# Kernel optimization log

Hardware: AMD Instinct MI355X
Metric: run time of the kernel (lower is better)

Reference implementation:

```python
import jax, jax.numpy as jnp
import numpy as np

B, N, E, D, H, C, FF, NQ, NCLS = 4, 1024, 512, 256, 2, 128, 1024, 4, 24
K_LOCAL, K_GLOBAL = 8, 7


def _ln(x, g, b, eps=1e-5):
    m = jnp.mean(x, -1, keepdims=True)
    v = jnp.mean((x - m) ** 2, -1, keepdims=True)
    return (x - m) * jax.lax.rsqrt(v + eps) * g + b


def _knn_mask(dist, k, exclude_self):
    # dist: [n, n]; returns bool mask[target, source] of k nearest sources per target
    n = dist.shape[-1]
    d = jnp.where(jnp.eye(n, dtype=bool), 1e9, dist) if exclude_self else dist
    idx = jax.lax.top_k(-d, k)[1]  # [n, k]
    rows = jnp.arange(n)[:, None]
    return jnp.zeros((n, n), dtype=bool).at[rows, idx].set(True)


def _mha(q, k, v, scale, extra_mask=None):
    # q: [B,Lq,H,C]  k,v: [B,Lk,H,C]
    logits = jnp.einsum('bqhc,bkhc->bhqk', q, k) * scale
    if extra_mask is not None:
        logits = logits + extra_mask
    a = jax.nn.softmax(logits, axis=-1)
    return jnp.einsum('bhqk,bkhc->bqhc', a, v)


def _forward(inputs, cellposes, sparse_rand, emb_W, emb_b, pe_tab, pe_W1, pe_b1, pe_W2, pe_b2,
             gat_W, gat_att_src, gat_att_dst, gat_b, ln_g, ln_b,
             tf_qkv_W, tf_qkv_b, tf_out_W, tf_out_b, tf_ff1_W, tf_ff1_b, tf_ff2_W, tf_ff2_b,
             tf_ln1_g, tf_ln1_b, tf_ln2_g, tf_ln2_b,
             query_embed, pool_in_W, pool_in_b, pool_out_W, pool_out_b,
             m1_W, m1_b, m_ln1_g, m_ln1_b, m2_W, m2_b, m_ln2_g, m_ln2_b, m3_W, m3_b,
             c1_W, c1_b, c2_W, c2_b, c3_W, c3_b, c4_W, c4_b, masks):
    # masks are all ones (full bags) -> key_padding_mask is all-False, no padding effect
    x = inputs @ emb_W.T + emb_b                                  # [B,N,D]
    # 2D position embedding: per-coordinate Embedding -> Linear -> ReLU -> Linear
    pos_idx = jnp.clip(cellposes, 0, 1000).astype(jnp.int32)      # [B,N,2]
    pes = []
    for c in range(2):
        e = pe_tab[c][pos_idx[..., c]]                            # [B,N,D//2]
        e = jax.nn.relu(e @ pe_W1[c].T + pe_b1[c]) @ pe_W2[c].T + pe_b2[c]
        pes.append(e)
    x = x + jnp.concatenate(pes, axis=-1)
    # kNN graph: local k=8 with self-loops + global k=7 without; coalesce('max') => edge-set union
    pm = cellposes.mean(axis=1, keepdims=True)
    ps = cellposes.std(axis=1, keepdims=True) + 1e-8
    pn = (cellposes - pm) / ps
    sq = jnp.sum((pn[:, :, None, :] - pn[:, None, :, :]) ** 2, axis=-1)
    dist = jax.lax.stop_gradient(jnp.sqrt(sq + 1e-12))            # [B,N,N]
    local = jax.vmap(lambda d: _knn_mask(d, K_LOCAL, False))(dist)
    glob = jax.vmap(lambda d: _knn_mask(d, K_GLOBAL, True))(dist)
    adj = local | glob                                            # [B, target, source]
    # GAT layers (PyG GATConv; edge weights are ignored since edge_dim=None)
    for l in range(gat_W.shape[0]):
        res = x
        h = (x @ gat_W[l].T).reshape(B, N, H, C)
        a_src = jnp.einsum('bnhc,hc->bnh', h, gat_att_src[l])
        a_dst = jnp.einsum('bnhc,hc->bnh', h, gat_att_dst[l])
        e = jax.nn.leaky_relu(a_dst[:, :, None, :] + a_src[:, None, :, :], 0.2)  # [B,t,s,H]
        e = jnp.where(adj[..., None], e, -1e9)
        a = jax.nn.softmax(e, axis=2)
        out = jnp.einsum('btsh,bshc->bthc', a, h).reshape(B, N, D) + gat_b[l]
        x = _ln(out + res, ln_g, ln_b)
    # TransformerEncoder: post-norm, ReLU FFN, batch_first, eval (no dropout)
    scale = 1.0 / jnp.sqrt(jnp.float32(C))
    for l in range(tf_qkv_W.shape[0]):
        qkv = x @ tf_qkv_W[l].T + tf_qkv_b[l]
        q, k, v = [t.reshape(B, N, H, C) for t in jnp.split(qkv, 3, axis=-1)]
        o = _mha(q, k, v, scale).reshape(B, N, D) @ tf_out_W[l].T + tf_out_b[l]
        x = _ln(x + o, tf_ln1_g[l], tf_ln1_b[l])
        ff = jax.nn.relu(x @ tf_ff1_W[l].T + tf_ff1_b[l]) @ tf_ff2_W[l].T + tf_ff2_b[l]
        x = _ln(x + ff, tf_ln2_g[l], tf_ln2_b[l])
    x = _ln(x, ln_g, ln_b)
    pooled_avg = x.mean(axis=1)                                   # AdaptiveAvgPool1d(1) == mean over seq
    # Sparse multihead attention pooling with learned queries
    queries = jnp.broadcast_to(query_embed[None], (B, NQ, D))
    attn_mask = jnp.where(sparse_rand < 0.3, 0.0, -1e9)           # [NQ, N]
    Wq, Wk, Wv = jnp.split(pool_in_W, 3, axis=0)
    bq, bk, bv = jnp.split(pool_in_b, 3, axis=0)
    q = (queries @ Wq.T + bq).reshape(B, NQ, H, C)
    k = (x @ Wk.T + bk).reshape(B, N, H, C)
    v = (x @ Wv.T + bv).reshape(B, N, H, C)
    pooled_att = _mha(q, k, v, scale, attn_mask[None, None]).reshape(B, NQ, D) @ pool_out_W.T + pool_out_b
    combined = jnp.concatenate([pooled_avg, pooled_att.reshape(B, NQ * D)], axis=-1)  # [B,(1+NQ)*D]
    h = jax.nn.relu(combined @ m1_W.T + m1_b)
    h = _ln(h, m_ln1_g, m_ln1_b)
    h = jax.nn.relu(h @ m2_W.T + m2_b)
    h = _ln(h, m_ln2_g, m_ln2_b)
    h = h @ m3_W.T + m3_b
    h = jax.nn.relu(h @ c1_W.T + c1_b)
    h = jax.nn.relu(h @ c2_W.T + c2_b)
    h = jax.nn.relu(h @ c3_W.T + c3_b)
    return h @ c4_W.T + c4_b                                      # [B, num_classes]


def setup_inputs() -> dict:
    key = jax.random.key(0)
    ks = iter(jax.random.split(key, 80))
    def W(shape, s=0.02):
        return jax.random.normal(next(ks), shape, jnp.float32) * s
    z = lambda *s: jnp.zeros(s, jnp.float32)
    o = lambda *s: jnp.ones(s, jnp.float32)
    return dict(
        inputs=jax.random.normal(next(ks), (B, N, E), jnp.float32),
        cellposes=jax.random.uniform(next(ks), (B, N, 2), jnp.float32) * 1000.0,
        sparse_rand=jax.random.uniform(next(ks), (NQ, N), jnp.float32),
        emb_W=W((D, E)), emb_b=z(D),
        pe_tab=W((2, 1001, D // 2)), pe_W1=W((2, D // 2, D // 2)), pe_b1=z(2, D // 2),
        pe_W2=W((2, D // 2, D // 2)), pe_b2=z(2, D // 2),
        gat_W=W((2, D, D)), gat_att_src=W((2, H, C)), gat_att_dst=W((2, H, C)), gat_b=z(2, D),
        ln_g=o(D), ln_b=z(D),
        tf_qkv_W=W((2, 3 * D, D)), tf_qkv_b=z(2, 3 * D), tf_out_W=W((2, D, D)), tf_out_b=z(2, D),
        tf_ff1_W=W((2, FF, D)), tf_ff1_b=z(2, FF), tf_ff2_W=W((2, D, FF)), tf_ff2_b=z(2, D),
        tf_ln1_g=o(2, D), tf_ln1_b=z(2, D), tf_ln2_g=o(2, D), tf_ln2_b=z(2, D),
        query_embed=W((NQ, D)),
        pool_in_W=W((3 * D, D)), pool_in_b=z(3 * D), pool_out_W=W((D, D)), pool_out_b=z(D),
        m1_W=W((1024, (1 + NQ) * D)), m1_b=z(1024), m_ln1_g=o(1024), m_ln1_b=z(1024),
        m2_W=W((1024, 1024)), m2_b=z(1024), m_ln2_g=o(1024), m_ln2_b=z(1024),
        m3_W=W((1024, 1024)), m3_b=z(1024),
        c1_W=W((1032, 1024)), c1_b=z(1032), c2_W=W((512, 1032)), c2_b=z(512),
        c3_W=W((256, 512)), c3_b=z(256), c4_W=W((NCLS, 256)), c4_b=z(NCLS),
        masks=jnp.ones((B, N), jnp.int32),
    )


def reference(inputs, cellposes, sparse_rand, emb_W, emb_b, pe_tab, pe_W1, pe_b1, pe_W2, pe_b2,
              gat_W, gat_att_src, gat_att_dst, gat_b, ln_g, ln_b,
              tf_qkv_W, tf_qkv_b, tf_out_W, tf_out_b, tf_ff1_W, tf_ff1_b, tf_ff2_W, tf_ff2_b,
              tf_ln1_g, tf_ln1_b, tf_ln2_g, tf_ln2_b,
              query_embed, pool_in_W, pool_in_b, pool_out_W, pool_out_b,
              m1_W, m1_b, m_ln1_g, m_ln1_b, m2_W, m2_b, m_ln2_g, m_ln2_b, m3_W, m3_b,
              c1_W, c1_b, c2_W, c2_b, c3_W, c3_b, c4_W, c4_b, masks):
    return _forward(inputs, cellposes, sparse_rand, emb_W, emb_b, pe_tab, pe_W1, pe_b1, pe_W2, pe_b2,
                    gat_W, gat_att_src, gat_att_dst, gat_b, ln_g, ln_b,
                    tf_qkv_W, tf_qkv_b, tf_out_W, tf_out_b, tf_ff1_W, tf_ff1_b, tf_ff2_W, tf_ff2_b,
                    tf_ln1_g, tf_ln1_b, tf_ln2_g, tf_ln2_b,
                    query_embed, pool_in_W, pool_in_b, pool_out_W, pool_out_b,
                    m1_W, m1_b, m_ln1_g, m_ln1_b, m2_W, m2_b, m_ln2_g, m_ln2_b, m3_W, m3_b,
                    c1_W, c1_b, c2_W, c2_b, c3_W, c3_b, c4_W, c4_b, masks)
```

## Files before the change

kernel.cpp:

```cpp
#include <hip/hip_runtime.h>
#include <hip/hip_bf16.h>


typedef __bf16 bf16x8 __attribute__((ext_vector_type(8)));
typedef float  f32x4  __attribute__((ext_vector_type(4)));

__device__ __forceinline__ ushort f2b(float f) {
  __hip_bfloat16 h = __float2bfloat16(f);
  return *(ushort*)&h;
}
__device__ __forceinline__ float b2f(ushort u) {
  union { unsigned i; float f; } v; v.i = ((unsigned)u) << 16; return v.f;
}

__device__ __forceinline__ float blk_sum256(float v, float* red) {
  int t = threadIdx.x;
  red[t] = v; __syncthreads();
  #pragma unroll
  for (int off = 128; off > 0; off >>= 1) {
    if (t < off) red[t] += red[t + off];
    __syncthreads();
  }
  float r = red[0]; __syncthreads();
  return r;
}

__device__ __forceinline__ void stage8(const ushort* __restrict__ src, ushort* dst) {
  *(uint4*)dst = *(const uint4*)src;
}
__device__ __forceinline__ void stage8(const float* __restrict__ src, ushort* dst) {
  float4 a = ((const float4*)src)[0];
  float4 b = ((const float4*)src)[1];
  ushort4 o0, o1;
  o0.x = f2b(a.x); o0.y = f2b(a.y); o0.z = f2b(a.z); o0.w = f2b(a.w);
  o1.x = f2b(b.x); o1.y = f2b(b.y); o1.z = f2b(b.z); o1.w = f2b(b.w);
  *(ushort4*)dst = o0;
  *(ushort4*)(dst + 4) = o1;
}

template<typename CT, typename AT, typename WT, bool VSPLIT, bool GATS>
__global__ __launch_bounds__(256) void mfma_gemm(
    const AT* __restrict__ A, int lda,
    const WT* __restrict__ Bw, int ldb,
    const float* __restrict__ bias,
    CT* __restrict__ C, int ldc, int K, int relu,
    ushort* __restrict__ VT,
    const float* __restrict__ asrcW, const float* __restrict__ adstW,
    float* __restrict__ ASRC, float* __restrict__ ADST)
{
  __shared__ ushort As[64][40];
  __shared__ ushort Bs[128][40];
  int tid = threadIdx.x;
  int lane = tid & 63, wave = tid >> 6;
  int wm = wave >> 1, wn = wave & 1;
  int quad = lane >> 4, l16 = lane & 15;
  long mBase = blockIdx.y * 64, nBase = blockIdx.x * 128;

  f32x4 zero4 = {0.f, 0.f, 0.f, 0.f};
  f32x4 acc[2][4];
  #pragma unroll
  for (int i = 0; i < 2; i++)
    #pragma unroll
    for (int j = 0; j < 4; j++) acc[i][j] = zero4;

  for (int k0 = 0; k0 < K; k0 += 32) {
    {
      int r = tid >> 2, sg = (tid & 3) * 8;
      stage8(A + (mBase + r) * lda + k0 + sg, &As[r][sg]);
    }
    #pragma unroll
    for (int p = 0; p < 2; p++) {
      int idx = p * 256 + tid;
      int r = idx >> 2, sg = (idx & 3) * 8;
      stage8(Bw + (nBase + r) * ldb + k0 + sg, &Bs[r][sg]);
    }
    __syncthreads();
    bf16x8 af[2], bfr[4];
    #pragma unroll
    for (int i = 0; i < 2; i++)
      af[i] = *(const bf16x8*)&As[wm * 32 + i * 16 + l16][quad * 8];
    #pragma unroll
    for (int j = 0; j < 4; j++)
      bfr[j] = *(const bf16x8*)&Bs[wn * 64 + j * 16 + l16][quad * 8];
    #pragma unroll
    for (int i = 0; i < 2; i++)
      #pragma unroll
      for (int j = 0; j < 4; j++)
        acc[i][j] = __builtin_amdgcn_mfma_f32_16x16x32_bf16(af[i], bfr[j], acc[i][j], 0, 0, 0);
    __syncthreads();
  }
  #pragma unroll
  for (int i = 0; i < 2; i++) {
    #pragma unroll
    for (int j = 0; j < 4; j++) {
      long col = nBase + wn * 64 + j * 16 + l16;
      float bv = bias ? bias[col] : 0.f;
      long row0 = mBase + wm * 32 + i * 16 + quad * 4;
      if (VSPLIT && col >= 512) {
        int cm = (int)col - 512, hh = cm >> 7, cc = cm & 127;
        long bidx = row0 >> 10, n0 = row0 & 1023;
        ushort4 o;
        o.x = f2b(acc[i][j][0] + bv);
        o.y = f2b(acc[i][j][1] + bv);
        o.z = f2b(acc[i][j][2] + bv);
        o.w = f2b(acc[i][j][3] + bv);
        *(ushort4*)&VT[(((bidx * 2 + hh) * 128 + cc) << 10) + n0] = o;
      } else {
        #pragma unroll
        for (int r = 0; r < 4; r++) {
          float v = acc[i][j][r] + bv;
          if (relu) v = fmaxf(v, 0.f);
          if constexpr (sizeof(CT) == 2) C[(row0 + r) * ldc + col] = f2b(v);
          else                           C[(row0 + r) * ldc + col] = v;
        }
      }
    }
  }
  if constexpr (GATS) {
    __shared__ float RS[64][2], RD[64][2];
    float ps[2][4], pd[2][4];
    #pragma unroll
    for (int i = 0; i < 2; i++)
      #pragma unroll
      for (int r = 0; r < 4; r++) { ps[i][r] = 0.f; pd[i][r] = 0.f; }
    #pragma unroll
    for (int j = 0; j < 4; j++) {
      long col = nBase + wn * 64 + j * 16 + l16;
      float ws = asrcW[col], wd = adstW[col];
      #pragma unroll
      for (int i = 0; i < 2; i++)
        #pragma unroll
        for (int r = 0; r < 4; r++) {
          ps[i][r] += acc[i][j][r] * ws;
          pd[i][r] += acc[i][j][r] * wd;
        }
    }
    #pragma unroll
    for (int off = 1; off < 16; off <<= 1)
      #pragma unroll
      for (int i = 0; i < 2; i++)
        #pragma unroll
        for (int r = 0; r < 4; r++) {
          ps[i][r] += __shfl_xor(ps[i][r], off);
          pd[i][r] += __shfl_xor(pd[i][r], off);
        }
    if (l16 == 0) {
      #pragma unroll
      for (int i = 0; i < 2; i++)
        #pragma unroll
        for (int r = 0; r < 4; r++) {
          int row = wm * 32 + i * 16 + quad * 4 + r;
          RS[row][wn] = ps[i][r];
          RD[row][wn] = pd[i][r];
        }
    }
    __syncthreads();
    if (tid < 64) {
      long gr = mBase + tid;
      ASRC[gr * 2 + blockIdx.x] = RS[tid][0] + RS[tid][1];
      ADST[gr * 2 + blockIdx.x] = RD[tid][0] + RD[tid][1];
    }
  }
}

template<typename CT, typename AT, typename WT>
static void mgemm(hipStream_t st, const AT* A, int lda, const WT* B, int ldb,
                  const float* bias, CT* C, int ldc, int M, int N, int K, int relu) {
  dim3 grid(N / 128, M / 64);
  mfma_gemm<CT, AT, WT, false, false><<<grid, 256, 0, st>>>(
      A, lda, B, ldb, bias, C, ldc, K, relu, nullptr, nullptr, nullptr, nullptr, nullptr);
}
template<typename AT, typename WT>
static void mgemm_vt(hipStream_t st, const AT* A, int lda, const WT* B, int ldb,
                     const float* bias, ushort* C, int ldc, int M, int N, int K, ushort* VT) {
  dim3 grid(N / 128, M / 64);
  mfma_gemm<ushort, AT, WT, true, false><<<grid, 256, 0, st>>>(
      A, lda, B, ldb, bias, C, ldc, K, 0, VT, nullptr, nullptr, nullptr, nullptr);
}
template<typename AT, typename WT>
static void mgemm_gat(hipStream_t st, const AT* A, int lda, const WT* B, int ldb,
                      float* C, int ldc, int M, int N, int K,
                      const float* asrcW, const float* adstW, float* AS, float* AD) {
  dim3 grid(N / 128, M / 64);
  mfma_gemm<float, AT, WT, false, true><<<grid, 256, 0, st>>>(
      A, lda, B, ldb, nullptr, C, ldc, K, 0, nullptr, asrcW, adstW, AS, AD);
}

__global__ __launch_bounds__(256) void pos_mlp(
    const float* __restrict__ cellp, const float* __restrict__ tab,
    const float* __restrict__ W1, const float* __restrict__ b1,
    const float* __restrict__ W2, const float* __restrict__ b2,
    float* __restrict__ X, ushort* __restrict__ Xb)
{
  __shared__ ushort Es[64][136];
  __shared__ ushort Bs[128][136];
  __shared__ ushort H1s[64][136];
  int tid = threadIdx.x;
  int lane = tid & 63, wave = tid >> 6;
  int wm = wave >> 1, wn = wave & 1;
  int quad = lane >> 4, l16 = lane & 15;
  int r0 = blockIdx.x * 64, c = blockIdx.y;

  #pragma unroll
  for (int p = 0; p < 4; p++) {
    int idx = p * 256 + tid;
    int r = idx >> 4, c8 = (idx & 15) * 8;
    float pos = cellp[(r0 + r) * 2 + c];
    pos = fminf(fmaxf(pos, 0.f), 1000.f);
    int pi = (int)pos;
    stage8(tab + ((long)(c * 1001 + pi)) * 128 + c8, &Es[r][c8]);
  }
  #pragma unroll
  for (int p = 0; p < 8; p++) {
    int idx = p * 256 + tid;
    int r = idx >> 4, c8 = (idx & 15) * 8;
    stage8(W1 + ((long)(c * 128 + r)) * 128 + c8, &Bs[r][c8]);
  }
  __syncthreads();

  f32x4 zero4 = {0.f, 0.f, 0.f, 0.f};
  f32x4 acc[2][4];
  #pragma unroll
  for (int i = 0; i < 2; i++)
    #pragma unroll
    for (int j = 0; j < 4; j++) acc[i][j] = zero4;
  #pragma unroll
  for (int ks = 0; ks < 4; ks++) {
    bf16x8 af[2], bfr[4];
    #pragma unroll
    for (int i = 0; i < 2; i++)
      af[i] = *(const bf16x8*)&Es[wm * 32 + i * 16 + l16][ks * 32 + quad * 8];
    #pragma unroll
    for (int j = 0; j < 4; j++)
      bfr[j] = *(const bf16x8*)&Bs[wn * 64 + j * 16 + l16][ks * 32 + quad * 8];
    #pragma unroll
    for (int i = 0; i < 2; i++)
      #pragma unroll
      for (int j = 0; j < 4; j++)
        acc[i][j] = __builtin_amdgcn_mfma_f32_16x16x32_bf16(af[i], bfr[j], acc[i][j], 0, 0, 0);
  }
  #pragma unroll
  for (int i = 0; i < 2; i++)
    #pragma unroll
    for (int j = 0; j < 4; j++) {
      int col = wn * 64 + j * 16 + l16;
      float bv = b1[c * 128 + col];
      #pragma unroll
      for (int r = 0; r < 4; r++) {
        int row = wm * 32 + i * 16 + quad * 4 + r;
        H1s[row][col] = f2b(fmaxf(acc[i][j][r] + bv, 0.f));
      }
    }
  __syncthreads();
  #pragma unroll
  for (int p = 0; p < 8; p++) {
    int idx = p * 256 + tid;
    int r = idx >> 4, c8 = (idx & 15) * 8;
    stage8(W2 + ((long)(c * 128 + r)) * 128 + c8, &Bs[r][c8]);
  }
  __syncthreads();
  #pragma unroll
  for (int i = 0; i < 2; i++)
    #pragma unroll
    for (int j = 0; j < 4; j++) acc[i][j] = zero4;
  #pragma unroll
  for (int ks = 0; ks < 4; ks++) {
    bf16x8 af[2], bfr[4];
    #pragma unroll
    for (int i = 0; i < 2; i++)
      af[i] = *(const bf16x8*)&H1s[wm * 32 + i * 16 + l16][ks * 32 + quad * 8];
    #pragma unroll
    for (int j = 0; j < 4; j++)
      bfr[j] = *(const bf16x8*)&Bs[wn * 64 + j * 16 + l16][ks * 32 + quad * 8];
    #pragma unroll
    for (int i = 0; i < 2; i++)
      #pragma unroll
      for (int j = 0; j < 4; j++)
        acc[i][j] = __builtin_amdgcn_mfma_f32_16x16x32_bf16(af[i], bfr[j], acc[i][j], 0, 0, 0);
  }
  #pragma unroll
  for (int i = 0; i < 2; i++)
    #pragma unroll
    for (int j = 0; j < 4; j++) {
      int col = wn * 64 + j * 16 + l16;
      float bv = b2[c * 128 + col];
      #pragma unroll
      for (int r = 0; r < 4; r++) {
        long row = r0 + wm * 32 + i * 16 + quad * 4 + r;
        long idx = row * 256 + c * 128 + col;
        float v = X[idx] + (acc[i][j][r] + bv);
        X[idx] = v;
        Xb[idx] = f2b(v);
      }
    }
}

template<int M_>
__global__ __launch_bounds__(256) void skinny_gemm(
    const float* __restrict__ A, int lda,
    const float* __restrict__ W, int K,
    float* __restrict__ P, int N, int slice)
{
  __shared__ float Asl[M_ * 192];
  __shared__ float Pr[4][M_][64];
  int tid = threadIdx.x;
  int ks = blockIdx.y;
  int kbeg = ks * slice;
  int kend = min(K, kbeg + slice);
  int sl = kend - kbeg;
  for (int idx = tid; idx < M_ * sl; idx += 256) {
    int m = idx / sl, k = idx - m * sl;
    Asl[m * sl + k] = A[(long)m * lda + kbeg + k];
  }
  __syncthreads();
  int n = blockIdx.x * 64 + (tid & 63);
  int sub = tid >> 6;
  int sl4 = (sl + 3) >> 2;
  int k0 = kbeg + sub * sl4;
  int k1 = min(kend, k0 + sl4);
  float acc[M_];
  #pragma unroll
  for (int m = 0; m < M_; m++) acc[m] = 0.f;
  if (n < N) {
    const float* wr = W + (long)n * K;
    for (int k = k0; k < k1; k++) {
      float w = wr[k];
      int kl = k - kbeg;
      #pragma unroll
      for (int m = 0; m < M_; m++) acc[m] += w * Asl[m * sl + kl];
    }
  }
  #pragma unroll
  for (int m = 0; m < M_; m++) Pr[sub][m][tid & 63] = acc[m];
  __syncthreads();
  if (sub == 0 && n < N) {
    #pragma unroll
    for (int m = 0; m < M_; m++) {
      float s = Pr[0][m][tid] + Pr[1][m][tid] + Pr[2][m][tid] + Pr[3][m][tid];
      P[((long)(ks * M_ + m)) * N + n] = s;
    }
  }
}

__global__ __launch_bounds__(256) void skinny_epi(
    const float* __restrict__ P, const float* __restrict__ bias,
    float* __restrict__ out, int M, int N, int KS, int relu)
{
  int idx = blockIdx.x * 256 + threadIdx.x;
  if (idx >= M * N) return;
  int m = idx / N, n = idx - m * N;
  float s = bias[n];
  for (int ks = 0; ks < KS; ks++) s += P[((long)(ks * M + m)) * N + n];
  if (relu) s = fmaxf(s, 0.f);
  out[(long)m * N + n] = s;
}

template<int M_>
static void sgemm(hipStream_t st, const float* A, int lda, const float* W, int K,
                  const float* bias, float* out, float* P, int N, int KS, int relu) {
  int slice = (K + KS - 1) / KS;
  dim3 grid((N + 63) / 64, KS);
  skinny_gemm<M_><<<grid, 256, 0, st>>>(A, lda, W, K, P, N, slice);
  skinny_epi<<<(M_ * N + 255) / 256, 256, 0, st>>>(P, bias, out, M_, N, KS, relu);
}

__global__ __launch_bounds__(256) void bag_stats(const float* __restrict__ cp, float* __restrict__ PN) {
  int b = blockIdx.x, tid = threadIdx.x;
  __shared__ float red[256];
  for (int c = 0; c < 2; c++) {
    float s = 0.f;
    for (int n = tid; n < 1024; n += 256) s += cp[((b << 10) + n) * 2 + c];
    float mean = blk_sum256(s, red) * (1.f / 1024.f);
    s = 0.f;
    for (int n = tid; n < 1024; n += 256) { float d = cp[((b << 10) + n) * 2 + c] - mean; s += d * d; }
    float var = blk_sum256(s, red) * (1.f / 1024.f);
    float inv = 1.f / (sqrtf(var) + 1e-8f);
    for (int n = tid; n < 1024; n += 256)
      PN[((b << 10) + n) * 2 + c] = (cp[((b << 10) + n) * 2 + c] - mean) * inv;
  }
}

__global__ __launch_bounds__(256) void knn_sel(const float* __restrict__ PN,
                                               int* __restrict__ NBR) {
  int blk = blockIdx.x;
  int b = blk >> 7, grp = blk & 127;
  int tid = threadIdx.x;
  int wave = tid >> 6, lane = tid & 63;
  __shared__ float px[1024], py[1024];
  for (int i = tid; i < 1024; i += 256) {
    px[i] = PN[((b << 10) + i) * 2 + 0];
    py[i] = PN[((b << 10) + i) * 2 + 1];
  }
  __syncthreads();
  #pragma unroll
  for (int sub = 0; sub < 2; sub++) {
    int t = grp * 8 + wave * 2 + sub;
    float tx = px[t], ty = py[t];
    float dloc[16];
    #pragma unroll
    for (int k = 0; k < 16; k++) {
      int s = lane + (k << 6);
      float dx = __fadd_rn(px[s], -tx), dy = __fadd_rn(py[s], -ty);
      float d2 = __fadd_rn(__fadd_rn(__fmul_rn(dx, dx), __fmul_rn(dy, dy)), 1e-12f);
      dloc[k] = sqrtf(d2);
    }
    int res[8];
    #pragma unroll
    for (int it = 0; it < 8; it++) {
      float bd = dloc[0]; int bk = 0;
      #pragma unroll
      for (int k = 1; k < 16; k++)
        if (dloc[k] < bd) { bd = dloc[k]; bk = k; }
      unsigned long long key =
          (((unsigned long long)__float_as_uint(bd)) << 32) | (unsigned)(lane + (bk << 6));
      #pragma unroll
      for (int off = 1; off < 64; off <<= 1) {
        unsigned long long o = __shfl_xor(key, off);
        if (o < key) key = o;
      }
      int widx = (int)(key & 0xffffffffu);
      res[it] = widx;
      if ((widx & 63) == lane) dloc[widx >> 6] = 3.4e38f;
    }
    if (lane < 8) NBR[((long)((b << 10) + t)) * 8 + lane] = res[lane];
  }
}

__global__ __launch_bounds__(256) void gat_aggr_ln(
    const float* __restrict__ Hh, const float* __restrict__ ASRC, const float* __restrict__ ADST,
    const int* __restrict__ NBR, const float* __restrict__ gbias,
    const float* __restrict__ lng, const float* __restrict__ lnb,
    float* __restrict__ X, ushort* __restrict__ Xb)
{
  int row = blockIdx.x, tid = threadIdx.x;
  int b = row >> 10;
  __shared__ int nb[8];
  __shared__ float w[2][8];
  __shared__ float red[256];
  if (tid < 8) {
    int v = NBR[(long)row * 8 + tid];
    nb[tid] = min(max(v, 0), 1023);
  }
  __syncthreads();
  if (tid < 16) {
    int i = tid & 7, h = tid >> 3;
    float e = ADST[row * 2 + h] + ASRC[((b << 10) + nb[i]) * 2 + h];
    w[h][i] = (e >= 0.f) ? e : 0.2f * e;
  }
  __syncthreads();
  if (tid < 2) {
    float m = -3.4e38f;
    for (int i = 0; i < 8; i++) m = fmaxf(m, w[tid][i]);
    float s = 0.f;
    for (int i = 0; i < 8; i++) { float e = expf(w[tid][i] - m); w[tid][i] = e; s += e; }
    float inv = 1.f / s;
    for (int i = 0; i < 8; i++) w[tid][i] *= inv;
  }
  __syncthreads();
  int h = tid >> 7, c = tid & 127;
  float acc = 0.f;
  #pragma unroll
  for (int i = 0; i < 8; i++)
    acc += w[h][i] * Hh[((long)((b << 10) + nb[i])) * 256 + h * 128 + c];
  float v = acc + gbias[tid] + X[(long)row * 256 + tid];
  float mean = blk_sum256(v, red) * (1.f / 256.f);
  float dv = v - mean;
  float var = blk_sum256(dv * dv, red) * (1.f / 256.f);
  float o = dv * rsqrtf(var + 1e-5f) * lng[tid] + lnb[tid];
  X[(long)row * 256 + tid] = o;
  Xb[(long)row * 256 + tid] = f2b(o);
}

__global__ __launch_bounds__(256) void add_ln4(const float* __restrict__ res,
    const float* __restrict__ Yv, const float* __restrict__ g, const float* __restrict__ b,
    float* __restrict__ out, ushort* __restrict__ outb)
{
  int wave = threadIdx.x >> 6, lane = threadIdx.x & 63;
  long row = blockIdx.x * 4 + wave;
  const float* yr = Yv + row * 256;
  const float* rr = res ? res + row * 256 : nullptr;
  float v[4];
  float s = 0.f;
  #pragma unroll
  for (int i = 0; i < 4; i++) {
    int d = lane + i * 64;
    float x = yr[d];
    if (rr) x += rr[d];
    v[i] = x; s += x;
  }
  #pragma unroll
  for (int off = 32; off > 0; off >>= 1) s += __shfl_xor(s, off);
  float mean = s * (1.f / 256.f);
  float vs = 0.f;
  #pragma unroll
  for (int i = 0; i < 4; i++) { float dv = v[i] - mean; vs += dv * dv; }
  #pragma unroll
  for (int off = 32; off > 0; off >>= 1) vs += __shfl_xor(vs, off);
  float rstd = rsqrtf(vs * (1.f / 256.f) + 1e-5f);
  #pragma unroll
  for (int i = 0; i < 4; i++) {
    int d = lane + i * 64;
    float o = (v[i] - mean) * rstd * g[d] + b[d];
    out[row * 256 + d] = o;
    if (outb) outb[row * 256 + d] = f2b(o);
  }
}

__global__ __launch_bounds__(256) void add_ln_big(const float* __restrict__ Yv,
    const float* __restrict__ g, const float* __restrict__ b,
    float* __restrict__ out)
{
  int row = blockIdx.x, tid = threadIdx.x;
  __shared__ float red[256];
  float vals[4];
  float s = 0.f;
  #pragma unroll
  for (int i = 0; i < 4; i++) {
    int d = tid + (i << 8);
    float v = Yv[(long)row * 1024 + d];
    vals[i] = v; s += v;
  }
  float mean = blk_sum256(s, red) * (1.f / 1024.f);
  s = 0.f;
  #pragma unroll
  for (int i = 0; i < 4; i++) { float dv = vals[i] - mean; s += dv * dv; }
  float var = blk_sum256(s, red) * (1.f / 1024.f);
  float rstd = rsqrtf(var + 1e-5f);
  #pragma unroll
  for (int i = 0; i < 4; i++) {
    int d = tid + (i << 8);
    out[(long)row * 1024 + d] = (vals[i] - mean) * rstd * g[d] + b[d];
  }
}

__global__ __launch_bounds__(256) void flash_mfma(const ushort* __restrict__ QKV,
                                                  const ushort* __restrict__ VT,
                                                  ushort* __restrict__ O)
{
  const float scale = 0.08838834764831845f;
  int blk = blockIdx.x;
  int qt = blk & 15, bh = blk >> 4;
  int b = bh >> 1, h = bh & 1;
  const ushort* qkg = QKV + (long)b * 1024 * 768 + h * 128;
  const ushort* vtg = VT + ((long)bh << 17);

  __shared__ ushort Qs[64][136];
  __shared__ ushort Ks[64][136];
  __shared__ ushort Vt[128][72];
  __shared__ ushort Ps[4][16][72];

  int tid = threadIdx.x;
  int wave = tid >> 6, lane = tid & 63;
  int quad = lane >> 4, l16 = lane & 15;

  #pragma unroll
  for (int p = 0; p < 4; p++) {
    int idx = p * 256 + tid;
    int r = idx >> 4, c8 = (idx & 15) * 8;
    *(uint4*)&Qs[r][c8] = *(const uint4*)(qkg + (long)(qt * 64 + r) * 768 + c8);
  }
  __syncthreads();
  bf16x8 af[4];
  #pragma unroll
  for (int ks = 0; ks < 4; ks++)
    af[ks] = *(const bf16x8*)&Qs[wave * 16 + l16][ks * 32 + quad * 8];

  f32x4 Oacc[8];
  f32x4 zero4 = {0.f, 0.f, 0.f, 0.f};
  #pragma unroll
  for (int j = 0; j < 8; j++) Oacc[j] = zero4;
  float mr[4], lr[4];
  #pragma unroll
  for (int r = 0; r < 4; r++) { mr[r] = -3.4e38f; lr[r] = 0.f; }

  for (int kt = 0; kt < 16; kt++) {
    __syncthreads();
    #pragma unroll
    for (int p = 0; p < 4; p++) {
      int idx = p * 256 + tid;
      int r = idx >> 4, c8 = (idx & 15) * 8;
      *(uint4*)&Ks[r][c8] = *(const uint4*)(qkg + (long)(kt * 64 + r) * 768 + 256 + c8);
      int c = idx >> 3, k8 = (idx & 7) * 8;
      *(uint4*)&Vt[c][k8] = *(const uint4*)(vtg + ((long)c << 10) + kt * 64 + k8);
    }
    __syncthreads();
    f32x4 acc[4];
    #pragma unroll
    for (int j = 0; j < 4; j++) acc[j] = zero4;
    #pragma unroll
    for (int ks = 0; ks < 4; ks++) {
      #pragma unroll
      for (int j = 0; j < 4; j++) {
        bf16x8 kb = *(const bf16x8*)&Ks[j * 16 + l16][ks * 32 + quad * 8];
        acc[j] = __builtin_amdgcn_mfma_f32_16x16x32_bf16(af[ks], kb, acc[j], 0, 0, 0);
      }
    }
    float sv[4][4], tmax[4];
    #pragma unroll
    for (int r = 0; r < 4; r++) tmax[r] = -3.4e38f;
    #pragma unroll
    for (int j = 0; j < 4; j++)
      #pragma unroll
      for (int r = 0; r < 4; r++) {
        float x = acc[j][r] * scale;
        sv[j][r] = x;
        tmax[r] = fmaxf(tmax[r], x);
      }
    #pragma unroll
    for (int off = 1; off < 16; off <<= 1)
      #pragma unroll
      for (int r = 0; r < 4; r++) tmax[r] = fmaxf(tmax[r], __shfl_xor(tmax[r], off));
    float alpha[4], rsum[4];
    #pragma unroll
    for (int r = 0; r < 4; r++) {
      float mn = fmaxf(mr[r], tmax[r]);
      alpha[r] = expf(mr[r] - mn);
      mr[r] = mn;
      rsum[r] = 0.f;
    }
    #pragma unroll
    for (int j = 0; j < 4; j++)
      #pragma unroll
      for (int r = 0; r < 4; r++) {
        float p = expf(sv[j][r] - mr[r]);
        sv[j][r] = p;
        rsum[r] += p;
      }
    #pragma unroll
    for (int off = 1; off < 16; off <<= 1)
      #pragma unroll
      for (int r = 0; r < 4; r++) rsum[r] += __shfl_xor(rsum[r], off);
    #pragma unroll
    for (int r = 0; r < 4; r++) lr[r] = lr[r] * alpha[r] + rsum[r];
    #pragma unroll
    for (int j = 0; j < 4; j++)
      #pragma unroll
      for (int r = 0; r < 4; r++)
        Ps[wave][quad * 4 + r][j * 16 + l16] = f2b(sv[j][r]);
    #pragma unroll
    for (int jj = 0; jj < 8; jj++)
      #pragma unroll
      for (int r = 0; r < 4; r++) Oacc[jj][r] *= alpha[r];
    __syncthreads();
    #pragma unroll
    for (int s = 0; s < 2; s++) {
      bf16x8 pa = *(const bf16x8*)&Ps[wave][l16][s * 32 + quad * 8];
      #pragma unroll
      for (int jj = 0; jj < 8; jj++) {
        bf16x8 vb = *(const bf16x8*)&Vt[jj * 16 + l16][s * 32 + quad * 8];
        Oacc[jj] = __builtin_amdgcn_mfma_f32_16x16x32_bf16(pa, vb, Oacc[jj], 0, 0, 0);
      }
    }
  }
  long row0 = (long)b * 1024 + qt * 64 + wave * 16 + quad * 4;
  #pragma unroll
  for (int jj = 0; jj < 8; jj++) {
    int col = h * 128 + jj * 16 + l16;
    #pragma unroll
    for (int r = 0; r < 4; r++)
      O[(row0 + r) * 256 + col] = f2b(Oacc[jj][r] / lr[r]);
  }
}

__global__ __launch_bounds__(128) void pool_split(
    const float* __restrict__ qe, const float* __restrict__ pinW, const float* __restrict__ pinB,
    const float* __restrict__ srand, const ushort* __restrict__ KV,
    float* __restrict__ PM, float* __restrict__ PL, float* __restrict__ PO)
{
  int cid = blockIdx.x;
  int id = blockIdx.y;
  int h = id & 1, nq = (id >> 1) & 3, b = id >> 3;
  int tid = threadIdx.x;
  __shared__ float qs[128];
  __shared__ float eg[128];
  __shared__ float red[128];
  {
    float a = pinB[h * 128 + tid];
    const float* wr = pinW + ((long)(h * 128 + tid)) * 256;
    const float* qr = qe + nq * 256;
    for (int i = 0; i < 256; i++) a += qr[i] * wr[i];
    qs[tid] = a;
  }
  __syncthreads();
  const float scale = 0.08838834764831845f;
  int s = cid * 128 + tid;
  float d = 0.f;
  {
    const ushort* kr = KV + ((long)((b << 10) + s)) * 512 + h * 128;
    #pragma unroll
    for (int c8 = 0; c8 < 128; c8 += 8) {
      uint4 kv4 = *(const uint4*)(kr + c8);
      const ushort* kp = (const ushort*)&kv4;
      #pragma unroll
      for (int j = 0; j < 8; j++) d += qs[c8 + j] * b2f(kp[j]);
    }
  }
  float lg = d * scale + ((srand[nq * 1024 + s] < 0.3f) ? 0.f : -1e9f);
  red[tid] = lg; __syncthreads();
  for (int off = 64; off > 0; off >>= 1) { if (tid < off) red[tid] = fmaxf(red[tid], red[tid + off]); __syncthreads(); }
  float m = red[0]; __syncthreads();
  float e = expf(lg - m);
  eg[tid] = e;
  red[tid] = e; __syncthreads();
  for (int off = 64; off > 0; off >>= 1) { if (tid < off) red[tid] += red[tid + off]; __syncthreads(); }
  float l = red[0];
  __syncthreads();
  float o = 0.f;
  const ushort* vbase = KV + ((long)((b << 10) + cid * 128)) * 512 + 256 + h * 128 + tid;
  for (int ss = 0; ss < 128; ss++)
    o += eg[ss] * b2f(vbase[(long)ss * 512]);
  int part = id * 8 + cid;
  PO[(long)part * 128 + tid] = o;
  if (tid == 0) { PM[part] = m; PL[part] = l; }
}

__global__ __launch_bounds__(128) void pool_merge(
    const float* __restrict__ PM, const float* __restrict__ PL, const float* __restrict__ PO,
    float* __restrict__ ATTP)
{
  int id = blockIdx.x;
  int h = id & 1, nq = (id >> 1) & 3, b = id >> 3;
  int tid = threadIdx.x;
  float m = -3.4e38f;
  #pragma unroll
  for (int c = 0; c < 8; c++) m = fmaxf(m, PM[id * 8 + c]);
  float l = 0.f, o = 0.f;
  #pragma unroll
  for (int c = 0; c < 8; c++) {
    float w = expf(PM[id * 8 + c] - m);
    l += PL[id * 8 + c] * w;
    o += PO[(long)(id * 8 + c) * 128 + tid] * w;
  }
  ATTP[(b * 4 + nq) * 256 + h * 128 + tid] = o / l;
}

__global__ __launch_bounds__(256) void col_mean_part(const float* __restrict__ X,
                                                     float* __restrict__ PSUM)
{
  int blk = blockIdx.x;
  int b = blk >> 4, ch = blk & 15;
  int d = threadIdx.x;
  float s = 0.f;
  int n0 = ch * 64;
  const float* xr = X + ((long)((b << 10) + n0)) * 256 + d;
  #pragma unroll 4
  for (int n = 0; n < 64; n++) s += xr[(long)n * 256];
  PSUM[(long)blk * 256 + d] = s;
}

__global__ __launch_bounds__(256) void combined_merge(const float* __restrict__ PSUM,
    const float* __restrict__ ATTO, float* __restrict__ CMB)
{
  int b = blockIdx.x, d = threadIdx.x;
  float s = 0.f;
  #pragma unroll
  for (int ch = 0; ch < 16; ch++) s += PSUM[(long)(b * 16 + ch) * 256 + d];
  CMB[b * 1280 + d] = s * (1.f / 1024.f);
  #pragma unroll
  for (int q = 0; q < 4; q++)
    CMB[b * 1280 + 256 + q * 256 + d] = ATTO[(b * 4 + q) * 256 + d];
}

__global__ void store_out(const float* __restrict__ src, float* __restrict__ dst, int n) {
  int i = blockIdx.x * blockDim.x + threadIdx.x;
  if (i < n) dst[i] = src[i];
}
__global__ void fill_out_zero(float* __restrict__ dst, int n) {
  int i = blockIdx.x * blockDim.x + threadIdx.x;
  if (i < n) dst[i] = 0.f;
}

extern "C" void kernel_launch(void* const* d_in, const int* in_sizes, int n_in,
                              void* d_out, int out_size, void* d_ws, size_t ws_size,
                              hipStream_t stream)
{
  const float* inp      = (const float*)d_in[0];
  const float* cellp    = (const float*)d_in[1];
  const float* srand    = (const float*)d_in[2];
  const float* emb_W    = (const float*)d_in[3];
  const float* emb_b    = (const float*)d_in[4];
  const float* pe_tab   = (const float*)d_in[5];
  const float* pe_W1    = (const float*)d_in[6];
  const float* pe_b1    = (const float*)d_in[7];
  const float* pe_W2    = (const float*)d_in[8];
  const float* pe_b2    = (const float*)d_in[9];
  const float* gat_W    = (const float*)d_in[10];
  const float* gat_asrc = (const float*)d_in[11];
  const float* gat_adst = (const float*)d_in[12];
  const float* gat_b    = (const float*)d_in[13];
  const float* ln_g     = (const float*)d_in[14];
  const float* ln_b     = (const float*)d_in[15];
  const float* qkv_W    = (const float*)d_in[16];
  const float* qkv_b    = (const float*)d_in[17];
  const float* out_W    = (const float*)d_in[18];
  const float* out_b    = (const float*)d_in[19];
  const float* ff1_W    = (const float*)d_in[20];
  const float* ff1_b    = (const float*)d_in[21];
  const float* ff2_W    = (const float*)d_in[22];
  const float* ff2_b    = (const float*)d_in[23];
  const float* ln1_g    = (const float*)d_in[24];
  const float* ln1_b    = (const float*)d_in[25];
  const float* ln2_g    = (const float*)d_in[26];
  const float* ln2_b    = (const float*)d_in[27];
  const float* q_emb    = (const float*)d_in[28];
  const float* pin_W    = (const float*)d_in[29];
  const float* pin_b    = (const float*)d_in[30];
  const float* pout_W   = (const float*)d_in[31];
  const float* pout_b   = (const float*)d_in[32];
  const float* m1_W     = (const float*)d_in[33];
  const float* m1_b     = (const float*)d_in[34];
  const float* mln1_g   = (const float*)d_in[35];
  const float* mln1_b   = (const float*)d_in[36];
  const float* m2_W     = (const float*)d_in[37];
  const float* m2_b     = (const float*)d_in[38];
  const float* mln2_g   = (const float*)d_in[39];
  const float* mln2_b   = (const float*)d_in[40];
  const float* m3_W     = (const float*)d_in[41];
  const float* m3_b     = (const float*)d_in[42];
  const float* c1_W     = (const float*)d_in[43];
  const float* c1_b     = (const float*)d_in[44];
  const float* c2_W     = (const float*)d_in[45];
  const float* c2_b     = (const float*)d_in[46];
  const float* c3_W     = (const float*)d_in[47];
  const float* c3_b     = (const float*)d_in[48];
  const float* c4_W     = (const float*)d_in[49];
  const float* c4_b     = (const float*)d_in[50];
  (void)in_sizes; (void)n_in;

  char* base = (char*)d_ws;
  size_t off = 0;
  auto alloc = [&](size_t bytes) { void* p = base + off; off += (bytes + 255) & ~size_t(255); return p; };
  float* PN    = (float*)alloc(32768);
  float* AS    = (float*)alloc(32768);
  float* AD    = (float*)alloc(32768);
  float* ATTP  = (float*)alloc(16384);
  float* ATTO  = (float*)alloc(16384);
  float* CMB   = (float*)alloc(20480);
  float* Ha    = (float*)alloc(16384);
  float* Hb    = (float*)alloc(16384);
  float* Hc    = (float*)alloc(16640);
  float* Hd    = (float*)alloc(8192);
  float* He    = (float*)alloc(4096);
  float* Hf    = (float*)alloc(512);
  float* Pk    = (float*)alloc(262144);
  float* PPM   = (float*)alloc(1024);
  float* PPL   = (float*)alloc(1024);
  float* PPO   = (float*)alloc(131072);
  float* PSUM  = (float*)alloc(65536);
  int*   NBR   = (int*)alloc(131072);
  float* X     = (float*)alloc(4194304);
  ushort* Xb   = (ushort*)alloc(2097152);
  char*  Rq    = (char*)alloc(6291456);
  char*  Rf    = (char*)alloc(4194304);
  float*  F1   = (float*)alloc(4194304);
  ushort* QKVb = (ushort*)Rq;
  float*  F2   = (float*)Rq;
  ushort* KVb  = (ushort*)Rq;
  ushort* Ob   = (ushort*)Rf;
  ushort* VT   = (ushort*)(Rf + 2097152);
  ushort* FFBb = (ushort*)Rf;
  if (ws_size < off) { fill_out_zero<<<1, 128, 0, stream>>>((float*)d_out, out_size); return; }

  bag_stats<<<4, 256, 0, stream>>>(cellp, PN);
  knn_sel<<<512, 256, 0, stream>>>(PN, NBR);

  mgemm<float>(stream, inp, 512, emb_W, 512, emb_b, X, 256, 4096, 256, 512, 0);
  pos_mlp<<<dim3(64, 2), 256, 0, stream>>>(cellp, pe_tab, pe_W1, pe_b1, pe_W2, pe_b2, X, Xb);

  for (int l = 0; l < 2; l++) {
    mgemm_gat(stream, Xb, 256, gat_W + l * 65536, 256, F1, 256, 4096, 256, 256,
              gat_asrc + l * 256, gat_adst + l * 256, AS, AD);
    gat_aggr_ln<<<4096, 256, 0, stream>>>(F1, AS, AD, NBR, gat_b + l * 256, ln_g, ln_b, X, Xb);
  }

  for (int l = 0; l < 2; l++) {
    mgemm_vt(stream, Xb, 256, qkv_W + (long)l * 768 * 256, 256, qkv_b + l * 768,
             QKVb, 768, 4096, 768, 256, VT);
    flash_mfma<<<256, 256, 0, stream>>>(QKVb, VT, Ob);
    mgemm<float>(stream, Ob, 256, out_W + l * 65536, 256, out_b + l * 256, F2, 256,
                 4096, 256, 256, 0);
    add_ln4<<<1024, 256, 0, stream>>>(X, F2, ln1_g + l * 256, ln1_b + l * 256, X, Xb);
    mgemm<ushort>(stream, Xb, 256, ff1_W + l * 262144, 256, ff1_b + l * 1024,
                  FFBb, 1024, 4096, 1024, 256, 1);
    mgemm<float>(stream, FFBb, 1024, ff2_W + l * 262144, 1024, ff2_b + l * 256,
                 F2, 256, 4096, 256, 1024, 0);
    add_ln4<<<1024, 256, 0, stream>>>(X, F2, ln2_g + l * 256, ln2_b + l * 256, X, Xb);
  }

  add_ln4<<<1024, 256, 0, stream>>>((const float*)nullptr, X, ln_g, ln_b, X, Xb);

  mgemm<ushort>(stream, Xb, 256, pin_W + 65536, 256, pin_b + 256, KVb, 512, 4096, 512, 256, 0);
  pool_split<<<dim3(8, 32), 128, 0, stream>>>(q_emb, pin_W, pin_b, srand, KVb, PPM, PPL, PPO);
  pool_merge<<<32, 128, 0, stream>>>(PPM, PPL, PPO, ATTP);
  sgemm<16>(stream, ATTP, 256, pout_W, 256, pout_b, ATTO, Pk, 256, 2, 0);
  col_mean_part<<<64, 256, 0, stream>>>(X, PSUM);
  combined_merge<<<4, 256, 0, stream>>>(PSUM, ATTO, CMB);

  sgemm<4>(stream, CMB, 1280, m1_W, 1280, m1_b, Ha, Pk, 1024, 8, 1);
  add_ln_big<<<4, 256, 0, stream>>>(Ha, mln1_g, mln1_b, Ha);
  sgemm<4>(stream, Ha, 1024, m2_W, 1024, m2_b, Hb, Pk, 1024, 8, 1);
  add_ln_big<<<4, 256, 0, stream>>>(Hb, mln2_g, mln2_b, Hb);
  sgemm<4>(stream, Hb, 1024, m3_W, 1024, m3_b, Ha, Pk, 1024, 8, 0);
  sgemm<4>(stream, Ha, 1024, c1_W, 1024, c1_b, Hc, Pk, 1032, 8, 1);
  sgemm<4>(stream, Hc, 1032, c2_W, 1032, c2_b, Hd, Pk, 512, 8, 1);
  sgemm<4>(stream, Hd, 512, c3_W, 512, c3_b, He, Pk, 256, 4, 1);
  sgemm<4>(stream, He, 256, c4_W, 256, c4_b, Hf, Pk, 24, 2, 0);
  store_out<<<1, 128, 0, stream>>>(Hf, (float*)d_out, out_size);
}
```

Measured before the change: 622.0 us.

## Prefetch K/V tiles into registers and trim flash attention grid to real heads

Flash attention now loads the next K and V tiles from global memory into registers while computing on the current tile. It then writes them to shared memory at points where the old data is no longer read: K after the score phase, V after the PV phase. This hides global-load latency behind MFMA work, at the cost of extra registers and an added barrier per iteration. The block-index mapping is reordered and the launch is reduced from 256 to 128 blocks. This matches the 8 batch-head pairs times 16 query tiles and drops redundant blocks that indexed past the batch.

```diff
diff --git a/kernel.cpp b/kernel.cpp
--- a/kernel.cpp
+++ b/kernel.cpp
@@ -539,7 +539,7 @@
 {
   const float scale = 0.08838834764831845f;
   int blk = blockIdx.x;
-  int qt = blk & 15, bh = blk >> 4;
+  int qt = blk >> 3, bh = blk & 7;
   int b = bh >> 1, h = bh & 1;
   const ushort* qkg = QKV + (long)b * 1024 * 768 + h * 128;
   const ushort* vtg = VT + ((long)bh << 17);
@@ -553,12 +553,29 @@
   int wave = tid >> 6, lane = tid & 63;
   int quad = lane >> 4, l16 = lane & 15;
 
+  uint4 kr[4], vr[4];
+  #pragma unroll
+  for (int p = 0; p < 4; p++) {
+    int idx = p * 256 + tid;
+    int r = idx >> 4, c8 = (idx & 15) * 8;
+    kr[p] = *(const uint4*)(qkg + (long)r * 768 + 256 + c8);
+    int c = idx >> 3, k8 = (idx & 7) * 8;
+    vr[p] = *(const uint4*)(vtg + ((long)c << 10) + k8);
+  }
   #pragma unroll
   for (int p = 0; p < 4; p++) {
     int idx = p * 256 + tid;
     int r = idx >> 4, c8 = (idx & 15) * 8;
     *(uint4*)&Qs[r][c8] = *(const uint4*)(qkg + (long)(qt * 64 + r) * 768 + c8);
   }
+  #pragma unroll
+  for (int p = 0; p < 4; p++) {
+    int idx = p * 256 + tid;
+    int r = idx >> 4, c8 = (idx & 15) * 8;
+    *(uint4*)&Ks[r][c8] = kr[p];
+    int c = idx >> 3, k8 = (idx & 7) * 8;
+    *(uint4*)&Vt[c][k8] = vr[p];
+  }
   __syncthreads();
   bf16x8 af[4];
   #pragma unroll
@@ -574,16 +591,16 @@
   for (int r = 0; r < 4; r++) { mr[r] = -3.4e38f; lr[r] = 0.f; }
 
   for (int kt = 0; kt < 16; kt++) {
-    __syncthreads();
-    #pragma unroll
-    for (int p = 0; p < 4; p++) {
-      int idx = p * 256 + tid;
-      int r = idx >> 4, c8 = (idx & 15) * 8;
-      *(uint4*)&Ks[r][c8] = *(const uint4*)(qkg + (long)(kt * 64 + r) * 768 + 256 + c8);
-      int c = idx >> 3, k8 = (idx & 7) * 8;
-      *(uint4*)&Vt[c][k8] = *(const uint4*)(vtg + ((long)c << 10) + kt * 64 + k8);
-    }
-    __syncthreads();
+    if (kt < 15) {
+      #pragma unroll
+      for (int p = 0; p < 4; p++) {
+        int idx = p * 256 + tid;
+        int r = idx >> 4, c8 = (idx & 15) * 8;
+        kr[p] = *(const uint4*)(qkg + (long)((kt + 1) * 64 + r) * 768 + 256 + c8);
+        int c = idx >> 3, k8 = (idx & 7) * 8;
+        vr[p] = *(const uint4*)(vtg + ((long)c << 10) + (kt + 1) * 64 + k8);
+      }
+    }
     f32x4 acc[4];
     #pragma unroll
     for (int j = 0; j < 4; j++) acc[j] = zero4;
@@ -642,6 +659,14 @@
       #pragma unroll
       for (int r = 0; r < 4; r++) Oacc[jj][r] *= alpha[r];
     __syncthreads();
+    if (kt < 15) {
+      #pragma unroll
+      for (int p = 0; p < 4; p++) {
+        int idx = p * 256 + tid;
+        int r = idx >> 4, c8 = (idx & 15) * 8;
+        *(uint4*)&Ks[r][c8] = kr[p];
+      }
+    }
     #pragma unroll
     for (int s = 0; s < 2; s++) {
       bf16x8 pa = *(const bf16x8*)&Ps[wave][l16][s * 32 + quad * 8];
@@ -651,6 +676,16 @@
         Oacc[jj] = __builtin_amdgcn_mfma_f32_16x16x32_bf16(pa, vb, Oacc[jj], 0, 0, 0);
       }
     }
+    __syncthreads();
+    if (kt < 15) {
+      #pragma unroll
+      for (int p = 0; p < 4; p++) {
+        int idx = p * 256 + tid;
+        int c = idx >> 3, k8 = (idx & 7) * 8;
+        *(uint4*)&Vt[c][k8] = vr[p];
+      }
+    }
+    __syncthreads();
   }
   long row0 = (long)b * 1024 + qt * 64 + wave * 16 + quad * 4;
   #pragma unroll
@@ -876,7 +911,7 @@
   for (int l = 0; l < 2; l++) {
     mgemm_vt(stream, Xb, 256, qkv_W + (long)l * 768 * 256, 256, qkv_b + l * 768,
              QKVb, 768, 4096, 768, 256, VT);
-    flash_mfma<<<256, 256, 0, stream>>>(QKVb, VT, Ob);
+    flash_mfma<<<128, 256, 0, stream>>>(QKVb, VT, Ob);
     mgemm<float>(stream, Ob, 256, out_W + l * 65536, 256, out_b + l * 256, F2, 256,
                  4096, 256, 256, 0);
     add_ln4<<<1024, 256, 0, stream>>>(X, F2, ln1_g + l * 256, ln1_b + l * 256, X, Xb);
```

New measurement: 654.2 us. 1.05x slower.

## Split flash attention over key halves and merge partial softmax results

Applied to the files above, without the earlier changes.

The attention kernel now gives each block half of the key range, so the 256-block grid covers all valid (batch, head, query-tile, half) combinations. A new merge kernel combines the two partial outputs using their running max and sum. The aim is to fill more compute units and shorten the per-block serial loop over key tiles. The cost is an extra kernel launch, global traffic for the partial results, and unnormalized partial outputs rounded to bf16 before the merge.

```diff
diff --git a/kernel.cpp b/kernel.cpp
--- a/kernel.cpp
+++ b/kernel.cpp
@@ -533,13 +533,16 @@
   }
 }
 
-__global__ __launch_bounds__(256) void flash_mfma(const ushort* __restrict__ QKV,
+__global__ __launch_bounds__(256) void flash_part(const ushort* __restrict__ QKV,
                                                   const ushort* __restrict__ VT,
-                                                  ushort* __restrict__ O)
+                                                  ushort* __restrict__ OP,
+                                                  float* __restrict__ Mp,
+                                                  float* __restrict__ Lp)
 {
   const float scale = 0.08838834764831845f;
   int blk = blockIdx.x;
-  int qt = blk & 15, bh = blk >> 4;
+  int bh = blk & 7, rest = blk >> 3;
+  int half = rest & 1, qt = rest >> 1;
   int b = bh >> 1, h = bh & 1;
   const ushort* qkg = QKV + (long)b * 1024 * 768 + h * 128;
   const ushort* vtg = VT + ((long)bh << 17);
@@ -573,7 +576,8 @@
   #pragma unroll
   for (int r = 0; r < 4; r++) { mr[r] = -3.4e38f; lr[r] = 0.f; }
 
-  for (int kt = 0; kt < 16; kt++) {
+  int kt0 = half * 8;
+  for (int kt = kt0; kt < kt0 + 8; kt++) {
     __syncthreads();
     #pragma unroll
     for (int p = 0; p < 4; p++) {
@@ -652,13 +656,50 @@
       }
     }
   }
-  long row0 = (long)b * 1024 + qt * 64 + wave * 16 + quad * 4;
+  long pbase = (long)blk * 64;
   #pragma unroll
   for (int jj = 0; jj < 8; jj++) {
-    int col = h * 128 + jj * 16 + l16;
-    #pragma unroll
-    for (int r = 0; r < 4; r++)
-      O[(row0 + r) * 256 + col] = f2b(Oacc[jj][r] / lr[r]);
+    int col = jj * 16 + l16;
+    #pragma unroll
+    for (int r = 0; r < 4; r++) {
+      int lrow = wave * 16 + quad * 4 + r;
+      OP[(pbase + lrow) * 128 + col] = f2b(Oacc[jj][r]);
+    }
+  }
+  if (l16 == 0) {
+    #pragma unroll
+    for (int r = 0; r < 4; r++) {
+      int lrow = wave * 16 + quad * 4 + r;
+      Mp[pbase + lrow] = mr[r];
+      Lp[pbase + lrow] = lr[r];
+    }
+  }
+}
+
+__global__ __launch_bounds__(256) void flash_merge(const ushort* __restrict__ OP,
+                                                   const float* __restrict__ Mp,
+                                                   const float* __restrict__ Lp,
+                                                   ushort* __restrict__ O)
+{
+  int blk = blockIdx.x;
+  int bh = blk & 7, qt = blk >> 3;
+  int b = bh >> 1, h = bh & 1;
+  int p0 = (qt * 2 + 0) * 8 + bh;
+  int p1 = (qt * 2 + 1) * 8 + bh;
+  int tid = threadIdx.x;
+  int r = tid >> 2, c0 = (tid & 3) * 32;
+  float m0 = Mp[p0 * 64 + r], m1 = Mp[p1 * 64 + r];
+  float l0 = Lp[p0 * 64 + r], l1 = Lp[p1 * 64 + r];
+  float mm = fmaxf(m0, m1);
+  float w0 = expf(m0 - mm), w1 = expf(m1 - mm);
+  float inv = 1.f / (w0 * l0 + w1 * l1);
+  const ushort* o0 = OP + ((long)(p0 * 64 + r)) * 128;
+  const ushort* o1 = OP + ((long)(p1 * 64 + r)) * 128;
+  ushort* od = O + ((long)(b * 1024 + qt * 64 + r)) * 256 + h * 128;
+  #pragma unroll 8
+  for (int c = c0; c < c0 + 32; c++) {
+    float o = w0 * b2f(o0[c]) + w1 * b2f(o1[c]);
+    od[c] = f2b(o * inv);
   }
 }
 
@@ -859,6 +900,9 @@
   ushort* Ob   = (ushort*)Rf;
   ushort* VT   = (ushort*)(Rf + 2097152);
   ushort* FFBb = (ushort*)Rf;
+  ushort* OPrt = (ushort*)F1;
+  float*  Mprt = Pk;
+  float*  Lprt = Pk + 16384;
   if (ws_size < off) { fill_out_zero<<<1, 128, 0, stream>>>((float*)d_out, out_size); return; }
 
   bag_stats<<<4, 256, 0, stream>>>(cellp, PN);
@@ -876,7 +920,8 @@
   for (int l = 0; l < 2; l++) {
     mgemm_vt(stream, Xb, 256, qkv_W + (long)l * 768 * 256, 256, qkv_b + l * 768,
              QKVb, 768, 4096, 768, 256, VT);
-    flash_mfma<<<256, 256, 0, stream>>>(QKVb, VT, Ob);
+    flash_part<<<256, 256, 0, stream>>>(QKVb, VT, OPrt, Mprt, Lprt);
+    flash_merge<<<128, 256, 0, stream>>>(OPrt, Mprt, Lprt, Ob);
     mgemm<float>(stream, Ob, 256, out_W + l * 65536, 256, out_b + l * 256, F2, 256,
                  4096, 256, 256, 0);
     add_ln4<<<1024, 256, 0, stream>>>(X, F2, ln1_g + l * 256, ln1_b + l * 256, X, Xb);
```

Result: no change. 613.8 us, median of 2 (-1.3%).
